# Optimization experiments

Hardware: AMD Instinct MI355X
Metric: run time of the kernel (lower is better)

The kernel has to match this reference:

```python
import jax, jax.numpy as jnp
import numpy as np
import functools

EPS_L1 = 1e-12   # torch F.normalize eps
BN_EPS = 1e-5    # torch BatchNorm eps


def _sga_dir(x, k, spatial_axis, reverse):
    """Semi-global aggregation along one spatial direction.
    x: [B,C,D,H,W] cost volume, k: [B,C,5,H,W] L1-normalized guidance weights.
    Recursion (GANet eq.4): A(p,d) = w0*C(p,d) + w1*A(p-r,d) + w2*A(p-r,d-1)
                                     + w3*A(p-r,d+1) + w4*max_d' A(p-r,d').
    Boundary pixel: A = C. d+-1 out of range treated as 0.
    """
    xm = jnp.moveaxis(x, spatial_axis, 0)   # [L, B,C,D,R]
    km = jnp.moveaxis(k, spatial_axis, 0)   # [L, B,C,5,R]
    if reverse:
        xm = xm[::-1]
        km = km[::-1]

    def step(prev, inp):
        # prev: [B,C,D,R]
        xw, kw = inp                                   # [B,C,D,R], [B,C,5,R]
        w0, w1, w2, w3, w4 = (kw[:, :, i, None, :] for i in range(5))  # [B,C,1,R]
        zero = jnp.zeros_like(prev[:, :, :1])
        prev_dm = jnp.concatenate([zero, prev[:, :, :-1]], axis=2)  # A(d-1)
        prev_dp = jnp.concatenate([prev[:, :, 1:], zero], axis=2)   # A(d+1)
        prev_mx = jnp.max(prev, axis=2, keepdims=True)              # max_d A
        out = w0 * xw + w1 * prev + w2 * prev_dm + w3 * prev_dp + w4 * prev_mx
        return out, out

    a0 = xm[0]
    _, rest = jax.lax.scan(step, a0, (xm[1:], km[1:]))
    out = jnp.concatenate([a0[None], rest], axis=0)
    if reverse:
        out = out[::-1]
    return jnp.moveaxis(out, 0, spatial_axis)


def _l1_normalize(k):
    # F.normalize(k, p=1, dim=2)
    s = jnp.sum(jnp.abs(k), axis=2, keepdims=True)
    return k / jnp.maximum(s, EPS_L1)


def _bn_eval(x, scale, bias):
    # eval-mode BatchNorm3d with running_mean=0, running_var=1
    inv = scale / jnp.sqrt(1.0 + BN_EPS)
    return x * inv[None, :, None, None, None] + bias[None, :, None, None, None]


def setup_inputs() -> dict:
    key = jax.random.key(0)
    k0, k1, k2 = jax.random.split(key, 3)
    B, C, D, H, W = 1, 32, 48, 64, 128
    x = jax.random.normal(k0, (B, C, D, H, W), dtype=jnp.float32)
    g = jax.random.normal(k1, (B, 4 * C * 5, H, W), dtype=jnp.float32)
    w_refine = jax.random.normal(k2, (C, C, 3, 3, 3), dtype=jnp.float32) * 0.05
    return {
        "x": x,
        "g": g,
        "w_refine": w_refine,
        "bn1_scale": jnp.ones((C,), jnp.float32),
        "bn1_bias": jnp.zeros((C,), jnp.float32),
        "bn2_scale": jnp.ones((C,), jnp.float32),
        "bn2_bias": jnp.zeros((C,), jnp.float32),
    }


def reference(x, g, w_refine, bn1_scale, bn1_bias, bn2_scale, bn2_bias):
    B, C, D, H, W = x.shape
    rem = x
    # split g into k1..k4, each [B,C,5,H,W], L1-normalize over the 5 weights
    kall = g.reshape(B, 4, C, 5, H, W)
    # directions: left->right, right->left (axis W=4), top->down, down->top (axis H=3)
    specs = [(4, False), (4, True), (3, False), (3, True)]
    outs = [
        _sga_dir(x, _l1_normalize(kall[:, i]), ax, rev)
        for i, (ax, rev) in enumerate(specs)
    ]
    agg = functools.reduce(jnp.maximum, outs)  # max over directions (GANet eq.5)
    # refine branch: BN -> ReLU -> Conv3d(3x3x3, no bias) -> BN
    y = jax.nn.relu(_bn_eval(agg, bn1_scale, bn1_bias))
    y = jax.lax.conv_general_dilated(
        y, w_refine, window_strides=(1, 1, 1), padding=[(1, 1)] * 3,
        dimension_numbers=("NCDHW", "OIDHW", "NCDHW"))
    y = _bn_eval(y, bn2_scale, bn2_bias)
    return jax.nn.relu(y + rem)
```

## Files before the change

kernel.cpp:

```cpp
#include <hip/hip_runtime.h>

#define C_ 32
#define D_ 48
#define H_ 64
#define W_ 128
#define HW_ 8192

using short8 = __attribute__((ext_vector_type(8))) short;
using half8  = __attribute__((ext_vector_type(8))) _Float16;
using half4  = __attribute__((ext_vector_type(4))) _Float16;
using half2v = __attribute__((ext_vector_type(2))) _Float16;
using f32x4  = __attribute__((ext_vector_type(4))) float;

__device__ __forceinline__ const unsigned short* uni_ptr(const unsigned short* p) {
    unsigned long long v = (unsigned long long)p;
    unsigned lo = __builtin_amdgcn_readfirstlane((unsigned)v);
    unsigned hi = __builtin_amdgcn_readfirstlane((unsigned)(v >> 32));
    return (const unsigned short*)(((unsigned long long)hi << 32) | lo);
}

__device__ __forceinline__ float dpp_shr1z(float v) {
    int r = __builtin_amdgcn_update_dpp(0, __builtin_bit_cast(int, v), 0x138, 0xf, 0xf, true);
    return __builtin_bit_cast(float, r);
}
__device__ __forceinline__ float dpp_shl1z(float v) {
    int r = __builtin_amdgcn_update_dpp(0, __builtin_bit_cast(int, v), 0x130, 0xf, 0xf, true);
    return __builtin_bit_cast(float, r);
}
__device__ __forceinline__ float wave_max48(float v) {
#define RMAX(ctrl)                                                                              \
    {                                                                                           \
        int t_ = __builtin_amdgcn_update_dpp(__builtin_bit_cast(int, v),                        \
                                             __builtin_bit_cast(int, v), ctrl, 0xf, 0xf, false);\
        v = fmaxf(v, __builtin_bit_cast(float, t_));                                            \
    }
    RMAX(0x111) RMAX(0x112) RMAX(0x114) RMAX(0x118) RMAX(0x142) RMAX(0x143)
#undef RMAX
    int m = __builtin_amdgcn_readlane(__builtin_bit_cast(int, v), 47);
    return __builtin_bit_cast(float, m);
}

__device__ __forceinline__ uint4 pack5(float c0, float c1, float c2, float c3, float c4) {
    float s = fabsf(c0) + fabsf(c1) + fabsf(c2) + fabsf(c3) + fabsf(c4);
    float rn = __builtin_amdgcn_rcpf(fmaxf(s, 1e-12f));
    unsigned h0 = __builtin_bit_cast(unsigned short, (_Float16)(c0 * rn));
    unsigned h1 = __builtin_bit_cast(unsigned short, (_Float16)(c1 * rn));
    unsigned h2 = __builtin_bit_cast(unsigned short, (_Float16)(c2 * rn));
    unsigned h3 = __builtin_bit_cast(unsigned short, (_Float16)(c3 * rn));
    unsigned h4 = __builtin_bit_cast(unsigned short, (_Float16)(c4 * rn));
    return uint4{h0 | (h1 << 16), h2 | (h3 << 16), h4, 0u};
}

__global__ __launch_bounds__(256) void k_front(const float* __restrict__ x,
                                               const float* __restrict__ g,
                                               const float* __restrict__ wr,
                                               _Float16* __restrict__ xtb,
                                               unsigned short* __restrict__ gq,
                                               _Float16* __restrict__ wt) {
    __shared__ float sbuf[10560];
    const int t = threadIdx.x;
    const int bid = blockIdx.x;
    if (bid < 2048) {
        const int c = bid >> 6, h = bid & 63;
        const float4* xb4 = (const float4*)(x + c * (D_ * HW_) + h * W_);
#pragma unroll
        for (int i = 0; i < 6; ++i) {
            int idx = i * 256 + t;
            int d = idx >> 5, wq = idx & 31;
            float4 v = xb4[d * 2048 + wq];
            sbuf[d * 129 + wq * 4 + 0] = v.x;
            sbuf[d * 129 + wq * 4 + 1] = v.y;
            sbuf[d * 129 + wq * 4 + 2] = v.z;
            sbuf[d * 129 + wq * 4 + 3] = v.w;
        }
        __syncthreads();
        half4* xo4 = (half4*)(xtb + ((c * H_ + h) * W_) * D_);
#pragma unroll
        for (int i = 0; i < 6; ++i) {
            int idx = i * 256 + t;
            int w = idx / 12, dq = idx - w * 12;
            half4 hv;
#pragma unroll
            for (int k = 0; k < 4; ++k) hv[k] = (_Float16)sbuf[(dq * 4 + k) * 129 + w];
            xo4[w * 12 + dq] = hv;
        }
    } else if (bid < 4096) {
        int e = (bid - 2048) * 256 + t;
        int dir = e >> 18;
        int c = (e >> 13) & 31;
        int pos = e & 8191;
        const float* gp = g + ((dir * C_ + c) * 5) * HW_ + pos;
        ((uint4*)gq)[e] = pack5(gp[0], gp[HW_], gp[2 * HW_], gp[3 * HW_], gp[4 * HW_]);
    } else if (bid < 4352) {
        int b = bid - 4096;
        int d2 = b >> 7, c = (b >> 2) & 31, w0 = (b & 3) * 32;
        const float* gp = g + (((d2 + 2) * C_ + c) * 5) * HW_;
#pragma unroll
        for (int k = 0; k < 40; ++k) {
            int j = k * 256 + t;
            int i = j >> 11, r = j & 2047;
            int h = r >> 5, wl = r & 31;
            sbuf[i * 2112 + h * 33 + wl] = gp[i * HW_ + h * W_ + w0 + wl];
        }
        __syncthreads();
        uint4* gqo = (uint4*)gq + ((d2 + 2) * C_ + c) * HW_;
#pragma unroll
        for (int k = 0; k < 8; ++k) {
            int j = k * 256 + t;
            int wl = j >> 6, h = j & 63;
            int s = h * 33 + wl;
            gqo[(w0 + wl) * 64 + h] = pack5(sbuf[s], sbuf[2112 + s], sbuf[4224 + s],
                                            sbuf[6336 + s], sbuf[8448 + s]);
        }
    } else {
        int idx = (bid - 4352) * 256 + t;
        int ci = idx & 31, co = (idx >> 5) & 31, tap = idx >> 10;
        wt[(tap * 32 + co) * 32 + ci] = (_Float16)wr[(co * 32 + ci) * 27 + tap];
    }
}

template <int T, int SS, bool REV>
__device__ __forceinline__ void scan_pass(const _Float16* __restrict__ xb,
                                          const unsigned short* __restrict__ gqb,
                                          _Float16* __restrict__ ab) {
    constexpr int PF = 8;
    _Float16 xs[PF], as[PF];
    half8 gs[PF];
    float prev;
    {
        constexpr int q0 = REV ? (T - 1) : 0;
        prev = (float)xb[q0 * SS];
        float o = prev;
        if (REV) o = fmaxf(o, (float)ab[q0 * SS]);
        ab[q0 * SS] = (_Float16)o;
    }
#pragma unroll
    for (int i = 0; i < PF; ++i) {
        int q = REV ? (T - 2 - i) : (1 + i);
        xs[i] = xb[q * SS];
        gs[i] = *(const half8*)(gqb + q * 8);
        if (REV) as[i] = ab[q * SS];
    }
    auto step = [&](int pc, int slot) {
        _Float16 xv = xs[slot];
        half8 gh = gs[slot];
        float av = REV ? (float)as[slot] : 0.f;
        int pn = pc + PF;
        if (pn < T) {
            int qn = REV ? (T - 1 - pn) : pn;
            xs[slot] = xb[qn * SS];
            gs[slot] = *(const half8*)(gqb + qn * 8);
            if (REV) as[slot] = ab[qn * SS];
        }
        float mx = wave_max48(prev);
        float dm = dpp_shr1z(prev);
        float dp = dpp_shl1z(prev);
        float a = fmaf((float)gh[0], (float)xv, 0.f);
        a = fmaf((float)gh[1], prev, a);
        a = fmaf((float)gh[2], dm, a);
        a = fmaf((float)gh[3], dp, a);
        a = fmaf((float)gh[4], mx, a);
        float o = REV ? fmaxf(a, av) : a;
        int qq = REV ? (T - 1 - pc) : pc;
        ab[qq * SS] = (_Float16)o;
        prev = a;
    };
    int p = 1;
#pragma unroll 1
    for (; p + PF <= T; p += PF) {
#pragma unroll
        for (int i = 0; i < PF; ++i) step(p + i, i);
    }
#pragma unroll
    for (int i = 0; i < PF; ++i)
        if (p + i < T) step(p + i, i);
}

__global__ __launch_bounds__(256) void k_scan(const _Float16* __restrict__ xtb,
                                              const unsigned short* __restrict__ gq,
                                              _Float16* __restrict__ agg1,
                                              _Float16* __restrict__ agg2) {
    const int lane = threadIdx.x & 63;
    const int wid = threadIdx.x >> 6;
    if (lane >= 48) return;
    if (blockIdx.x < 512) {
        const int L = blockIdx.x * 4 + wid;
        const int c = L >> 6, h = L & 63;
        const int base = ((c * H_ + h) * W_) * D_ + lane;
        const _Float16* xb = xtb + base;
        _Float16* ab = agg1 + base;
        const unsigned short* g0 = uni_ptr(gq + (unsigned)((0 * C_ + c) * HW_ + h * W_) * 8);
        const unsigned short* g1 = uni_ptr(gq + (unsigned)((1 * C_ + c) * HW_ + h * W_) * 8);
        scan_pass<W_, D_, false>(xb, g0, ab);
        __builtin_amdgcn_s_waitcnt(0);
        scan_pass<W_, D_, true>(xb, g1, ab);
    } else {
        const int L = (blockIdx.x - 512) * 4 + wid;
        const int c = L >> 7, w = L & 127;
        const int base = (c * HW_ + w) * D_ + lane;
        const _Float16* xb = xtb + base;
        _Float16* ab = agg2 + base;
        const unsigned short* g2 = uni_ptr(gq + (unsigned)((2 * C_ + c) * HW_ + w * H_) * 8);
        const unsigned short* g3 = uni_ptr(gq + (unsigned)((3 * C_ + c) * HW_ + w * H_) * 8);
        scan_pass<H_, W_ * D_, false>(xb, g2, ab);
        __builtin_amdgcn_s_waitcnt(0);
        scan_pass<H_, W_ * D_, true>(xb, g3, ab);
    }
}

__global__ __launch_bounds__(256) void k_prep(const _Float16* __restrict__ agg1,
                                              const _Float16* __restrict__ agg2,
                                              const float* __restrict__ bn1s,
                                              const float* __restrict__ bn1b,
                                              _Float16* __restrict__ y2p) {
    const int t = threadIdx.x;
    if (blockIdx.x >= 1024) {
        int i = (blockIdx.x - 1024) * 256 + t;
        if (i < 143136) {
            unsigned u4i;
            if (i < 52000) {
                int slab = i / 26000, off = i % 26000;
                u4i = slab * 65 * 26000 + off;
            } else if (i < 118560) {
                int j = i - 52000;
                int h = j / 1040 + 1, r = j % 1040;
                int d = (r < 520) ? 0 : 49, off = (r < 520) ? r : r - 520;
                u4i = h * 26000 + d * 520 + off;
            } else {
                int j = i - 118560;
                int h = j / 384 + 1, r = j % 384;
                int d = (r >> 3) + 1, r2 = r & 7;
                int w = (r2 >> 2) ? 129 : 0;
                u4i = h * 26000 + d * 520 + w * 4 + (r2 & 3);
            }
            ((uint4*)y2p)[u4i] = uint4{0u, 0u, 0u, 0u};
        }
        return;
    }
    __shared__ float L[48 * 33];
    __shared__ float s_inv[32], s_b[32];
    if (t < 32) {
        s_inv[t] = bn1s[t] * rsqrtf(1.f + 1e-5f);
        s_b[t] = bn1b[t];
    }
    __syncthreads();
    const int h = blockIdx.x >> 4;
    const int w0 = (blockIdx.x & 15) * 8;
    const half4* a14 = (const half4*)agg1;
    const half4* a24 = (const half4*)agg2;
    for (int wi = 0; wi < 8; ++wi) {
        int w = w0 + wi;
        for (int i = t; i < 384; i += 256) {
            int c = i / 12, dq = i - c * 12;
            int ao = ((c * H_ + h) * W_ + w) * 12 + dq;
            half4 u1 = a14[ao];
            half4 u2 = a24[ao];
            float si = s_inv[c], sb = s_b[c];
#pragma unroll
            for (int k = 0; k < 4; ++k) {
                float v = fmaxf((float)u1[k], (float)u2[k]);
                L[(dq * 4 + k) * 33 + c] = fmaxf(v * si + sb, 0.f);
            }
        }
        __syncthreads();
        half2v* yb2 = (half2v*)y2p;
#pragma unroll
        for (int i = 0; i < 3; ++i) {
            int idx = i * 256 + t;
            int c2 = idx & 15, d = idx >> 4;
            half2v hv;
            hv[0] = (_Float16)L[d * 33 + c2 * 2];
            hv[1] = (_Float16)L[d * 33 + c2 * 2 + 1];
            yb2[(((h + 1) * 50 + (d + 1)) * 130 + (w + 1)) * 16 + c2] = hv;
        }
        __syncthreads();
    }
}

__global__ __launch_bounds__(256, 3) void k_conv(const _Float16* __restrict__ y2p,
                                                 const _Float16* __restrict__ wt,
                                                 const float* __restrict__ x,
                                                 const float* __restrict__ bn2s,
                                                 const float* __restrict__ bn2b,
                                                 float* __restrict__ out) {
    __shared__ __align__(16) unsigned short ls[24576];
    const int t = threadIdx.x;
    const int lane = t & 63, wid = t >> 6;
    const int h = blockIdx.x >> 5;
    const int ow = ((blockIdx.x >> 2) & 7) * 16;
    const int od = (blockIdx.x & 3) * 12;
    {
        const int j0 = wid * 12;
#pragma unroll
        for (int jj = 0; jj < 12; ++jj) {
            int j = j0 + jj;
            int i = j * 64 + lane;
            int seg = i / 72, off = i - seg * 72;
            int kh = seg / 14, dz = seg - kh * 14;
            const _Float16* gp = y2p + (unsigned)(((h + kh) * 50 + od + dz) * 520 + ow * 4 + off) * 8;
            if (i < 3024)
                __builtin_amdgcn_global_load_lds(
                    (const __attribute__((address_space(1))) void*)gp,
                    (__attribute__((address_space(3))) void*)(ls + (unsigned)j * 512), 16, 0, 0);
        }
    }
    __syncthreads();
    const int n = lane & 15, kg = lane >> 4;
    const int dd0 = wid * 3;
    f32x4 acc[3][2] = {};
#pragma unroll
    for (int kh = 0; kh < 3; ++kh)
#pragma unroll
        for (int kd = 0; kd < 3; ++kd)
#pragma unroll
            for (int kw = 0; kw < 3; ++kw) {
                int tap = (kd * 3 + kh) * 3 + kw;
                half8 A0 = *(const half8*)(wt + (tap * 32 + n) * 32 + kg * 8);
                half8 A1 = *(const half8*)(wt + (tap * 32 + 16 + n) * 32 + kg * 8);
                const unsigned short* bp =
                    ls + (kh * 14 + dd0 + kd) * 576 + (n + kw) * 32 + kg * 8;
#pragma unroll
                for (int dd = 0; dd < 3; ++dd) {
                    half8 b = __builtin_bit_cast(half8, *(const short8*)(bp + dd * 576));
                    acc[dd][0] = __builtin_amdgcn_mfma_f32_16x16x32_f16(A0, b, acc[dd][0], 0, 0, 0);
                    acc[dd][1] = __builtin_amdgcn_mfma_f32_16x16x32_f16(A1, b, acc[dd][1], 0, 0, 0);
                }
            }
    const float rs = rsqrtf(1.f + 1e-5f);
#pragma unroll
    for (int ct = 0; ct < 2; ++ct)
#pragma unroll
        for (int r = 0; r < 4; ++r) {
            int co = ct * 16 + kg * 4 + r;
            float sc = bn2s[co] * rs, bi = bn2b[co];
#pragma unroll
            for (int dd = 0; dd < 3; ++dd) {
                int d = od + dd0 + dd;
                int addr = ((co * D_ + d) * H_ + h) * W_ + ow + n;
                float val = acc[dd][ct][r] * sc + bi;
                out[addr] = fmaxf(val + x[addr], 0.f);
            }
        }
}

extern "C" void kernel_launch(void* const* d_in, const int* in_sizes, int n_in,
                              void* d_out, int out_size, void* d_ws, size_t ws_size,
                              hipStream_t stream) {
    const float* x = (const float*)d_in[0];
    const float* g = (const float*)d_in[1];
    const float* wr = (const float*)d_in[2];
    const float* bn1s = (const float*)d_in[3];
    const float* bn1b = (const float*)d_in[4];
    const float* bn2s = (const float*)d_in[5];
    const float* bn2b = (const float*)d_in[6];
    float* out = (float*)d_out;
    char* ws = (char*)d_ws;

    _Float16* xtb = (_Float16*)ws;
    _Float16* y2p = (_Float16*)ws;
    _Float16* agg1 = (_Float16*)(ws + 33554432);
    _Float16* agg2 = (_Float16*)(ws + 58720256);
    unsigned short* gq = (unsigned short*)(ws + 83886080);
    _Float16* wt = (_Float16*)(ws + 100663296);

    k_front<<<4460, 256, 0, stream>>>(x, g, wr, xtb, gq, wt);
    k_scan<<<1536, 256, 0, stream>>>(xtb, gq, agg1, agg2);
    k_prep<<<1584, 256, 0, stream>>>(agg1, agg2, bn1s, bn1b, y2p);
    k_conv<<<2048, 256, 0, stream>>>(y2p, wt, x, bn2s, bn2b, out);
}
```

Measured before the change: 277.7 us.

## Fuse forward and reverse SGA scans into one packed-half2 interleaved pass

Runs the forward and reverse scan directions together in one loop. The two recurrent states are packed into a single half2 register, so one set of DPP shifts and one wave-max reduction serves both directions. This roughly halves the serial dependency chain of cross-lane ops per output and drops the separate second pass. In the second half, each direction combines with the other's stored value via max. The cost is that the neighbor and max inputs to the recurrence are now rounded to fp16 (round-toward-zero) instead of kept in fp32, which may reduce accuracy.

```diff
diff --git a/kernel.cpp b/kernel.cpp
--- a/kernel.cpp
+++ b/kernel.cpp
@@ -19,25 +19,29 @@
     return (const unsigned short*)(((unsigned long long)hi << 32) | lo);
 }
 
-__device__ __forceinline__ float dpp_shr1z(float v) {
-    int r = __builtin_amdgcn_update_dpp(0, __builtin_bit_cast(int, v), 0x138, 0xf, 0xf, true);
-    return __builtin_bit_cast(float, r);
-}
-__device__ __forceinline__ float dpp_shl1z(float v) {
-    int r = __builtin_amdgcn_update_dpp(0, __builtin_bit_cast(int, v), 0x130, 0xf, 0xf, true);
-    return __builtin_bit_cast(float, r);
-}
-__device__ __forceinline__ float wave_max48(float v) {
-#define RMAX(ctrl)                                                                              \
-    {                                                                                           \
-        int t_ = __builtin_amdgcn_update_dpp(__builtin_bit_cast(int, v),                        \
-                                             __builtin_bit_cast(int, v), ctrl, 0xf, 0xf, false);\
-        v = fmaxf(v, __builtin_bit_cast(float, t_));                                            \
-    }
-    RMAX(0x111) RMAX(0x112) RMAX(0x114) RMAX(0x118) RMAX(0x142) RMAX(0x143)
-#undef RMAX
-    int m = __builtin_amdgcn_readlane(__builtin_bit_cast(int, v), 47);
-    return __builtin_bit_cast(float, m);
+__device__ __forceinline__ int dpp_shr1z_pk(int v) {
+    return __builtin_amdgcn_update_dpp(0, v, 0x138, 0xf, 0xf, true);
+}
+__device__ __forceinline__ int dpp_shl1z_pk(int v) {
+    return __builtin_amdgcn_update_dpp(0, v, 0x130, 0xf, 0xf, true);
+}
+__device__ __forceinline__ int wave_max48_pk(int v) {
+#define RMAXP(ctrl)                                                                   \
+    {                                                                                 \
+        int t_ = __builtin_amdgcn_update_dpp(v, v, ctrl, 0xf, 0xf, false);            \
+        half2v a_ = __builtin_bit_cast(half2v, v);                                    \
+        half2v b_ = __builtin_bit_cast(half2v, t_);                                   \
+        half2v m_ = __builtin_elementwise_max(a_, b_);                                \
+        v = __builtin_bit_cast(int, m_);                                              \
+    }
+    RMAXP(0x111) RMAXP(0x112) RMAXP(0x114) RMAXP(0x118) RMAXP(0x142) RMAXP(0x143)
+#undef RMAXP
+    return __builtin_amdgcn_readlane(v, 47);
+}
+
+__device__ __forceinline__ int pack_rtz(float a, float b) {
+    auto r = __builtin_amdgcn_cvt_pkrtz(a, b);
+    return __builtin_bit_cast(int, r);
 }
 
 __device__ __forceinline__ uint4 pack5(float c0, float c1, float c2, float c3, float c4) {
@@ -119,61 +123,106 @@
     }
 }
 
-template <int T, int SS, bool REV>
-__device__ __forceinline__ void scan_pass(const _Float16* __restrict__ xb,
-                                          const unsigned short* __restrict__ gqb,
-                                          _Float16* __restrict__ ab) {
+template <int T, int SS>
+__device__ __forceinline__ void scan_fused(const _Float16* __restrict__ xb,
+                                           const unsigned short* __restrict__ gF,
+                                           const unsigned short* __restrict__ gR,
+                                           _Float16* __restrict__ ab) {
     constexpr int PF = 8;
-    _Float16 xs[PF], as[PF];
-    half8 gs[PF];
-    float prev;
+    constexpr int M1 = T / 2 - 1;
+    _Float16 xF[PF], xR[PF], aFc[PF], aRc[PF];
+    half8 gFs[PF], gRs[PF];
+    float pF = (float)xb[0];
+    float pR = (float)xb[(T - 1) * SS];
+    int pk = pack_rtz(pF, pR);
     {
-        constexpr int q0 = REV ? (T - 1) : 0;
-        prev = (float)xb[q0 * SS];
-        float o = prev;
-        if (REV) o = fmaxf(o, (float)ab[q0 * SS]);
-        ab[q0 * SS] = (_Float16)o;
+        half2v ph = __builtin_bit_cast(half2v, pk);
+        ab[0] = ph[0];
+        ab[(T - 1) * SS] = ph[1];
     }
 #pragma unroll
     for (int i = 0; i < PF; ++i) {
-        int q = REV ? (T - 2 - i) : (1 + i);
-        xs[i] = xb[q * SS];
-        gs[i] = *(const half8*)(gqb + q * 8);
-        if (REV) as[i] = ab[q * SS];
-    }
-    auto step = [&](int pc, int slot) {
-        _Float16 xv = xs[slot];
-        half8 gh = gs[slot];
-        float av = REV ? (float)as[slot] : 0.f;
-        int pn = pc + PF;
-        if (pn < T) {
-            int qn = REV ? (T - 1 - pn) : pn;
-            xs[slot] = xb[qn * SS];
-            gs[slot] = *(const half8*)(gqb + qn * 8);
-            if (REV) as[slot] = ab[qn * SS];
-        }
-        float mx = wave_max48(prev);
-        float dm = dpp_shr1z(prev);
-        float dp = dpp_shl1z(prev);
-        float a = fmaf((float)gh[0], (float)xv, 0.f);
-        a = fmaf((float)gh[1], prev, a);
-        a = fmaf((float)gh[2], dm, a);
-        a = fmaf((float)gh[3], dp, a);
-        a = fmaf((float)gh[4], mx, a);
-        float o = REV ? fmaxf(a, av) : a;
-        int qq = REV ? (T - 1 - pc) : pc;
-        ab[qq * SS] = (_Float16)o;
-        prev = a;
+        int p = 1 + i, q = T - 2 - i;
+        xF[i] = xb[p * SS];
+        gFs[i] = *(const half8*)(gF + p * 8);
+        xR[i] = xb[q * SS];
+        gRs[i] = *(const half8*)(gR + q * 8);
+    }
+    auto step = [&](int s, bool comb) {
+        const int slot = (s - 1) & (PF - 1);
+        const int p = s, q = T - 1 - s;
+        _Float16 xFv = xF[slot];
+        half8 ghF = gFs[slot];
+        _Float16 xRv = xR[slot];
+        half8 ghR = gRs[slot];
+        float avF = 0.f, avR = 0.f;
+        if (comb) {
+            avF = (float)aFc[slot];
+            avR = (float)aRc[slot];
+        }
+        int pn = s + PF;
+        if (pn <= T - 1) {
+            int qn = T - 1 - pn;
+            xF[slot] = xb[pn * SS];
+            gFs[slot] = *(const half8*)(gF + pn * 8);
+            xR[slot] = xb[qn * SS];
+            gRs[slot] = *(const half8*)(gR + qn * 8);
+            if (comb) {
+                aFc[slot] = ab[pn * SS];
+                aRc[slot] = ab[qn * SS];
+            }
+        }
+        int mxpk = wave_max48_pk(pk);
+        int dmpk = dpp_shr1z_pk(pk);
+        int dppk = dpp_shl1z_pk(pk);
+        half2v mx = __builtin_bit_cast(half2v, mxpk);
+        half2v dm = __builtin_bit_cast(half2v, dmpk);
+        half2v dp = __builtin_bit_cast(half2v, dppk);
+        float aFv = fmaf((float)ghF[0], (float)xFv, 0.f);
+        aFv = fmaf((float)ghF[1], pF, aFv);
+        aFv = fmaf((float)ghF[2], (float)dm[0], aFv);
+        aFv = fmaf((float)ghF[3], (float)dp[0], aFv);
+        aFv = fmaf((float)ghF[4], (float)mx[0], aFv);
+        float aRv = fmaf((float)ghR[0], (float)xRv, 0.f);
+        aRv = fmaf((float)ghR[1], pR, aRv);
+        aRv = fmaf((float)ghR[2], (float)dm[1], aRv);
+        aRv = fmaf((float)ghR[3], (float)dp[1], aRv);
+        aRv = fmaf((float)ghR[4], (float)mx[1], aRv);
+        pF = aFv;
+        pR = aRv;
+        pk = pack_rtz(pF, pR);
+        if (comb) {
+            ab[p * SS] = (_Float16)fmaxf(aFv, avF);
+            ab[q * SS] = (_Float16)fmaxf(aRv, avR);
+        } else {
+            half2v ph = __builtin_bit_cast(half2v, pk);
+            ab[p * SS] = ph[0];
+            ab[q * SS] = ph[1];
+        }
     };
-    int p = 1;
+    int s = 1;
 #pragma unroll 1
-    for (; p + PF <= T; p += PF) {
-#pragma unroll
-        for (int i = 0; i < PF; ++i) step(p + i, i);
-    }
+    for (; s + PF <= M1 + 1; s += PF)
+#pragma unroll
+        for (int i = 0; i < PF; ++i) step(s + i, false);
 #pragma unroll
     for (int i = 0; i < PF; ++i)
-        if (p + i < T) step(p + i, i);
+        if (s + i <= M1) step(s + i, false);
+    s = M1 + 1;
+    __builtin_amdgcn_s_waitcnt(0);
+#pragma unroll
+    for (int i = 0; i < PF; ++i) {
+        int ps = M1 + 1 + i;
+        aFc[(ps - 1) & (PF - 1)] = ab[ps * SS];
+        aRc[(ps - 1) & (PF - 1)] = ab[(T - 1 - ps) * SS];
+    }
+#pragma unroll 1
+    for (; s + PF <= T; s += PF)
+#pragma unroll
+        for (int i = 0; i < PF; ++i) step(s + i, true);
+#pragma unroll
+    for (int i = 0; i < PF; ++i)
+        if (s + i <= T - 1) step(s + i, true);
 }
 
 __global__ __launch_bounds__(256) void k_scan(const _Float16* __restrict__ xtb,
@@ -187,24 +236,16 @@
         const int L = blockIdx.x * 4 + wid;
         const int c = L >> 6, h = L & 63;
         const int base = ((c * H_ + h) * W_) * D_ + lane;
-        const _Float16* xb = xtb + base;
-        _Float16* ab = agg1 + base;
         const unsigned short* g0 = uni_ptr(gq + (unsigned)((0 * C_ + c) * HW_ + h * W_) * 8);
         const unsigned short* g1 = uni_ptr(gq + (unsigned)((1 * C_ + c) * HW_ + h * W_) * 8);
-        scan_pass<W_, D_, false>(xb, g0, ab);
-        __builtin_amdgcn_s_waitcnt(0);
-        scan_pass<W_, D_, true>(xb, g1, ab);
+        scan_fused<W_, D_>(xtb + base, g0, g1, agg1 + base);
     } else {
         const int L = (blockIdx.x - 512) * 4 + wid;
         const int c = L >> 7, w = L & 127;
         const int base = (c * HW_ + w) * D_ + lane;
-        const _Float16* xb = xtb + base;
-        _Float16* ab = agg2 + base;
         const unsigned short* g2 = uni_ptr(gq + (unsigned)((2 * C_ + c) * HW_ + w * H_) * 8);
         const unsigned short* g3 = uni_ptr(gq + (unsigned)((3 * C_ + c) * HW_ + w * H_) * 8);
-        scan_pass<H_, W_ * D_, false>(xb, g2, ab);
-        __builtin_amdgcn_s_waitcnt(0);
-        scan_pass<H_, W_ * D_, true>(xb, g3, ab);
+        scan_fused<H_, W_ * D_>(xtb + base, g2, g3, agg2 + base);
     }
 }
 
```

Result: slower. 319.9 us (+15.2%).
